# Performance work log

Hardware: AMD Instinct MI355X
Metric: run time of the kernel (lower is better)

Reference implementation:

```python
import jax, jax.numpy as jnp
import numpy as np

B, T, C = 4, 1024, 1024
N = 64          # head_size
H = C // N      # 16 heads
DW, DA, DV, DG = 64, 64, 64, 160


def setup_inputs() -> dict:
    key = jax.random.key(0)
    ks = iter(jax.random.split(key, 40))
    rn = lambda shape, s=1.0: jax.random.normal(next(ks), shape, dtype=jnp.float32) * s
    ru = lambda shape: jax.random.uniform(next(ks), shape, dtype=jnp.float32)
    cs = 0.5 / (C ** 0.5)
    return {
        "x": rn((B, T, C)),
        "v_first": rn((B, T, C)),
        "x_r": ru((1, 1, C)), "x_w": ru((1, 1, C)), "x_k": ru((1, 1, C)),
        "x_v": ru((1, 1, C)), "x_a": ru((1, 1, C)), "x_g": ru((1, 1, C)),
        "w0": rn((1, 1, C), 0.3) - 1.0,
        "w1": rn((C, DW), 0.05), "w2": rn((DW, C), 0.05),
        "a0": rn((1, 1, C), 0.3) - 0.19,
        "a1": rn((C, DA), 0.05), "a2": rn((DA, C), 0.05),
        "v0": rn((1, 1, C), 0.3) + 0.73,
        "v1": rn((C, DV), 0.05), "v2": rn((DV, C), 0.05),
        "g1": rn((C, DG), 0.05), "g2": rn((DG, C), 0.05),
        "k_k": ru((1, 1, C)) * 0.2 + 0.6,
        "k_a": ru((1, 1, C)) * 0.2 + 0.9,
        "r_k": rn((H, N), 0.05) - 0.04,
        "Wr": rn((C, C), cs), "Wk": rn((C, C), 0.1 * cs),
        "Wv": rn((C, C), cs), "Wo": rn((C, C), 0.02),
        "gn_w": jnp.ones((C,), jnp.float32), "gn_b": jnp.zeros((C,), jnp.float32),
        "ln_w": jnp.ones((C,), jnp.float32), "ln_b": jnp.zeros((C,), jnp.float32),
    }


def reference(x, v_first, x_r, x_w, x_k, x_v, x_a, x_g,
              w0, w1, w2, a0, a1, a2, v0, v1, v2, g1, g2,
              k_k, k_a, r_k, Wr, Wk, Wv, Wo, gn_w, gn_b, ln_w, ln_b):
    Bb, Tt, Cc = x.shape
    # ZeroPad2d((0,0,1,-1)): shift tokens right by one along T, then subtract x
    xx = jnp.concatenate([jnp.zeros_like(x[:, :1]), x[:, :-1]], axis=1) - x
    xr = x + xx * x_r; xw = x + xx * x_w; xkk = x + xx * x_k
    xv = x + xx * x_v; xa = x + xx * x_a; xg = x + xx * x_g

    r = xr @ Wr.T                                                    # [B,T,C]
    w = -jax.nn.softplus(-(w0 + jnp.tanh(xw @ w1) @ w2)) - 0.5       # log-decay <= -0.5
    k = xkk @ Wk.T
    v = xv @ Wv.T
    # layer_id=1 != 0 -> value residual mixing with v_first
    v = v + (v_first - v) * jax.nn.sigmoid(v0 + (xv @ v1) @ v2)
    a = jax.nn.sigmoid(a0 + (xa @ a1) @ a2)
    g = jax.nn.sigmoid(xg @ g1) @ g2

    kk = (k * k_k).reshape(Bb, Tt, H, N)
    kk = kk / jnp.maximum(jnp.linalg.norm(kk, axis=-1, keepdims=True), 1e-12)
    kk = kk.reshape(Bb, Tt, Cc)
    k = k * (1.0 + (a - 1.0) * k_a)

    # RWKV-7 generalized delta rule scan: kernel args (r, w, k, v, -kk, kk*a)
    decay = jnp.exp(-jnp.exp(w))                                     # [B,T,C]
    aa = -kk
    bb = kk * a
    tbhn = lambda t: t.reshape(Bb, Tt, H, N).transpose(1, 0, 2, 3)   # [T,B,H,N]
    rs, ws, ks_, vs, as_, bs = map(tbhn, (r, decay, k, v, aa, bb))

    S0 = jnp.zeros((Bb, H, N, N), dtype=x.dtype)  # [B,H, value N, key N]

    def step(S, inp):
        r_t, w_t, k_t, v_t, a_t, b_t = inp
        sa = jnp.einsum('bhij,bhj->bhi', S, a_t)                     # removal readout
        S = (S * w_t[:, :, None, :]
             + sa[..., None] * b_t[:, :, None, :]
             + v_t[..., None] * k_t[:, :, None, :])
        y = jnp.einsum('bhij,bhj->bhi', S, r_t)
        return S, (y, sa)

    _, (ys, sas) = jax.lax.scan(step, S0, (rs, ws, ks_, vs, as_, bs))
    x_att = ys.transpose(1, 0, 2, 3).reshape(Bb, Tt, Cc)
    sa_out = sas.transpose(1, 0, 2, 3).reshape(Bb, Tt, Cc)

    # ln_sa: LayerNorm over C (eps 1e-5)
    mu = sa_out.mean(-1, keepdims=True)
    var = sa_out.var(-1, keepdims=True)
    state_rep = (sa_out - mu) / jnp.sqrt(var + 1e-5) * ln_w + ln_b

    # ln_x: GroupNorm(H groups, eps=0.00064) applied per token
    xh = x_att.reshape(Bb, Tt, H, N)
    gm = xh.mean(-1, keepdims=True)
    gv = xh.var(-1, keepdims=True)
    xn = ((xh - gm) / jnp.sqrt(gv + 0.00064)).reshape(Bb, Tt, Cc) * gn_w + gn_b

    rh = r.reshape(Bb, Tt, H, N)
    kh = k.reshape(Bb, Tt, H, N)
    vh = v.reshape(Bb, Tt, H, N)
    bonus = ((rh * kh * r_k).sum(-1, keepdims=True) * vh).reshape(Bb, Tt, Cc)
    x_att = xn + bonus

    out = (x_att * g) @ Wo.T
    return out, v_first, state_rep
```

## Files before the change

### kernel.cpp

```cpp
#include <hip/hip_runtime.h>
#include <hip/hip_bf16.h>
#include <cstdint>
#include <cstddef>

typedef __attribute__((ext_vector_type(8))) short short8;
typedef __attribute__((ext_vector_type(4))) short short4v;
typedef __attribute__((ext_vector_type(4))) float f32x4;

#define DEVINL static __device__ __forceinline__

DEVINL float b2f(unsigned short u) {
    union { unsigned int i; float f; } v; v.i = ((unsigned int)u) << 16; return v.f;
}
DEVINL unsigned short f2bh(float f) {
    __hip_bfloat16 h = __float2bfloat16(f);
    union { __hip_bfloat16 h; unsigned short u; } v; v.h = h; return v.u;
}
DEVINL unsigned short f2b(float f) { return f2bh(f); }
DEVINL void cv8(short8 h, f32x4& lo, f32x4& hi) {
    #pragma unroll
    for (int j = 0; j < 4; ++j) {
        lo[j] = b2f((unsigned short)h[j]);
        hi[j] = b2f((unsigned short)h[j + 4]);
    }
}
DEVINL void cv4(short4v h, f32x4& o) {
    #pragma unroll
    for (int j = 0; j < 4; ++j) o[j] = b2f((unsigned short)h[j]);
}
DEVINL void stage16(const unsigned short* g, unsigned short* l) {
    __builtin_amdgcn_global_load_lds(
        (const __attribute__((address_space(1))) unsigned int*)g,
        (__attribute__((address_space(3))) unsigned int*)l,
        16, 0, 0);
}
DEVINL void xcd_swz(int& bx, int& by) {
    int id = by * 32 + bx;
    int k = id & 7, m = id >> 3;
    bx = 4 * k + (m & 3);
    by = m >> 2;
}

static constexpr int Bsz = 4, Tn = 1024, Cn = 1024, Hn = 16, Nn = 64;
static constexpr int Mrows = Bsz * Tn;
static constexpr size_t MX = (size_t)Mrows * Cn;
static constexpr int NCHUNK = 16, CL = 64;
static constexpr int DLD = 65;

__global__ __launch_bounds__(256) void k_prep_all(
    const float* __restrict__ x,
    const float* __restrict__ mr, const float* __restrict__ mw,
    const float* __restrict__ mk, const float* __restrict__ mv,
    const float* __restrict__ ma, const float* __restrict__ mg,
    unsigned short* __restrict__ xr, unsigned short* __restrict__ xw,
    unsigned short* __restrict__ xk, unsigned short* __restrict__ xv,
    unsigned short* __restrict__ xa, unsigned short* __restrict__ xg,
    const float* __restrict__ Wr, const float* __restrict__ Wk,
    const float* __restrict__ Wv, const float* __restrict__ Wo,
    unsigned short* __restrict__ WrB, unsigned short* __restrict__ WkB,
    unsigned short* __restrict__ WvB, unsigned short* __restrict__ WoB,
    const float* __restrict__ w1, const float* __restrict__ w2,
    const float* __restrict__ a1, const float* __restrict__ a2,
    const float* __restrict__ v1, const float* __restrict__ v2,
    const float* __restrict__ g1, const float* __restrict__ g2,
    unsigned short* __restrict__ w1T, unsigned short* __restrict__ w2T,
    unsigned short* __restrict__ a1T, unsigned short* __restrict__ a2T,
    unsigned short* __restrict__ v1T, unsigned short* __restrict__ v2T,
    unsigned short* __restrict__ g1T, unsigned short* __restrict__ g2T)
{
    const int bx = blockIdx.x;
    const int tid = threadIdx.x;
    if (bx < 2048) {
        size_t e = ((size_t)bx * 256 + tid) * 8;
        int c = (int)(e & (Cn - 1));
        int t = (int)((e >> 10) & (Tn - 1));
        float xf[8], d[8];
        {
            f32x4 x0 = *(const f32x4*)(x + e);
// ... 205 lines not shown
    if (b < 48) { zz = b >> 4; bxi = b & 15; byi = 0; }
    else        { zz = 3; int r = b - 48; bxi = r & 15; byi = r >> 4; }
    const unsigned short* A = (zz == 0) ? Aw : (zz == 1) ? Aa : (zz == 2) ? Avv : Ag;
    const unsigned short* Bt = (zz == 0) ? Bw1 : (zz == 1) ? Ba1 : (zz == 2) ? Bv1 : Bg1;
    const int N = (zz == 3) ? 160 : 64;
    const int tid = threadIdx.x, wid = tid >> 6, lane = tid & 63;
    const int r16 = lane & 15, k8 = (lane >> 4) * 8;
    const int m0 = bxi * 256 + wid * 64;
    const int n0 = byi * 64;
    f32x4 acc[4][4];
    #pragma unroll
    for (int a = 0; a < 4; ++a)
        #pragma unroll
        for (int bb = 0; bb < 4; ++bb) acc[a][bb] = (f32x4){0.f, 0.f, 0.f, 0.f};
    gemm_core(A, Cn, Bt, Cn, m0, n0, N, Cn, r16, k8, acc);
    if (zz == 0)      gemm_epi<1, 0>(acc, m0, n0, N, 64,  nullptr, Dw, nullptr, lane);
    else if (zz == 1) gemm_epi<0, 0>(acc, m0, n0, N, 64,  nullptr, Da, nullptr, lane);
    else if (zz == 2) gemm_epi<0, 0>(acc, m0, n0, N, 64,  nullptr, Dvh, nullptr, lane);
    else              gemm_epi<2, 0>(acc, m0, n0, N, 160, nullptr, Dg, nullptr, lane);
}

__global__ __launch_bounds__(256) void gemm_s2(
    const unsigned short* __restrict__ hw, const unsigned short* __restrict__ ha,
    const unsigned short* __restrict__ hv, const unsigned short* __restrict__ hg,
    const unsigned short* __restrict__ w2T, const unsigned short* __restrict__ a2T,
    const unsigned short* __restrict__ v2T, const unsigned short* __restrict__ g2T,
    float* __restrict__ Wdec, unsigned short* __restrict__ Ab,
    unsigned short* __restrict__ SVb, unsigned short* __restrict__ Gb,
    const float* __restrict__ w0, const float* __restrict__ a0,
    const float* __restrict__ v0)
{
    const int z = blockIdx.z;
    int bxs = blockIdx.x, bys = blockIdx.y;
    xcd_swz(bxs, bys);
    const int m0 = bxs * 128, n0 = bys * 128;
    if (z == 0)
        gemm_lds_body<4, 1>(hw, 64, w2T, 64, Wdec, nullptr, Cn, w0, 64, m0, n0);
    else if (z == 1)
        gemm_lds_body<3, 0>(ha, 64, a2T, 64, nullptr, Ab, Cn, a0, 64, m0, n0);
    else if (z == 2)
        gemm_lds_body<3, 0>(hv, 64, v2T, 64, nullptr, SVb, Cn, v0, 64, m0, n0);
    else
        gemm_lds_body<0, 0>(hg, 160, g2T, 160, nullptr, Gb, Cn, nullptr, 160, m0, n0);
}

__global__ __launch_bounds__(1024, 1) void kA_wy(
    const float* __restrict__ Wp,
    unsigned short* __restrict__ Kp,
    unsigned short* __restrict__ Vp,
    const unsigned short* __restrict__ SVp,
    unsigned short* __restrict__ Aap,
    const float* __restrict__ vfirst,
    const float* __restrict__ kkw, const float* __restrict__ kaw,
    float* __restrict__ Pg,
    float* __restrict__ Cg,
    float* __restrict__ Qg,
    float* __restrict__ SAp)
{
    __shared__ float Dl[64 * DLD];
    __shared__ float Lf[64 * 72];
    __shared__ float Xf[64 * 132];
    __shared__ unsigned short ah[64 * 72], al[64 * 72];
    __shared__ unsigned short bh_[64 * 72], bl_[64 * 72];
    __shared__ unsigned short kh[64 * 72], kl[64 * 72];
    __shared__ unsigned short vt[64 * 72];
    __shared__ unsigned short sc[64 * 72];
    __shared__ float dT[64];

    const int tid = threadIdx.x;
    const int bx = blockIdx.x;
    const int bhd = bx >> 4, cc = bx & 15;
    const size_t base0 = ((size_t)(bhd >> 4) * Tn + (size_t)cc * CL) * Cn + (size_t)(bhd & 15) * Nn;
    const size_t mb = (size_t)bx * 4096;

    {
        const int t = tid >> 4, s4 = (tid & 15) * 4;
        const size_t g = base0 + (size_t)t * Cn + s4;
        const int ch = (bhd & 15) * Nn + s4;

        f32x4 kv, av, vv, sv;
        cv4(*(const short4v*)(Kp + g), kv);
        cv4(*(const short4v*)(Aap + g), av);
        cv4(*(const short4v*)(Vp + g), vv);
        cv4(*(const short4v*)(SVp + g), sv);
        f32x4 kkwv = *(const f32x4*)(kkw + ch);
        f32x4 kawv = *(const f32x4*)(kaw + ch);
        f32x4 vfv  = *(const f32x4*)(vfirst + g);

        f32x4 kkv = kv * kkwv;
        f32x4 sq = kkv * kkv;
        float s = sq[0] + sq[1] + sq[2] + sq[3];
        s += __shfl_xor(s, 1, 64); s += __shfl_xor(s, 2, 64);
        s += __shfl_xor(s, 4, 64); s += __shfl_xor(s, 8, 64);
        float inv = 1.f / fmaxf(sqrtf(s), 1e-12f);

        short4v o_a, o_b, o_k, o_v;
        #pragma unroll
        for (int j = 0; j < 4; ++j) {
            float kkx = kkv[j] * inv;
            o_a[j] = (short)f2b(-kkx);
            o_b[j] = (short)f2b(kkx * av[j]);
            float kf = kv[j] * (1.f + (av[j] - 1.f) * kawv[j]);
            o_k[j] = (short)f2b(kf);
            float vf = vv[j] + (vfv[j] - vv[j]) * sv[j];
            o_v[j] = (short)f2b(vf);
        }
        *(short4v*)&ah[t * 72 + s4] = o_a;
        *(short4v*)&bh_[t * 72 + s4] = o_b;
        *(short4v*)&kh[t * 72 + s4] = o_k;
// ... 109 lines not shown
        for (int jj = 0; jj < 4; ++jj)
            Xf[t * 132 + s4 + jj] = b2f(ah[t * 72 + s4 + jj]) + b2f(al[t * 72 + s4 + jj]);
    }
    {
        f32x4 acc = (f32x4){0.f, 0.f, 0.f, 0.f};
        #pragma unroll
        for (int ks = 0; ks < 2; ++ks) {
            short8 Af = *(const short8*)&sc[(rt * 16 + r16) * 72 + ks * 32 + kg * 8];
            short8 Bf = *(const short8*)&vt[(ct * 16 + r16) * 72 + ks * 32 + kg * 8];
            acc = __builtin_amdgcn_mfma_f32_16x16x32_bf16(Af, Bf, acc, 0, 0, 0);
        }
        #pragma unroll
        for (int r = 0; r < 4; ++r)
            Xf[(rt * 16 + kg * 4 + r) * 132 + 64 + ct * 16 + r16] = acc[r];
    }
    __syncthreads();

    for (int bi = 0; bi < 4; ++bi) {
        if (bi > 0) {
            const int c = tid & 127;
            const int rb = tid >> 7;
            const int t0 = bi * 16 + rb * 2;
            float a0 = Xf[t0 * 132 + c];
            float a1 = Xf[(t0 + 1) * 132 + c];
            for (int s = 0; s < bi * 16; ++s) {
                float xv = Xf[s * 132 + c];
                a0 += Lf[t0 * 72 + s] * xv;
                a1 += Lf[(t0 + 1) * 72 + s] * xv;
            }
            Xf[t0 * 132 + c] = a0;
            Xf[(t0 + 1) * 132 + c] = a1;
            __syncthreads();
        }
        if (w < 2) {
            const int c = w * 64 + lane;
            float xcol[16];
            #pragma unroll
            for (int u = 0; u < 16; ++u) xcol[u] = Xf[(bi * 16 + u) * 132 + c];
            for (int rr = 1; rr < 16; ++rr) {
                float a2 = xcol[rr];
                for (int s = 0; s < rr; ++s)
                    a2 += Lf[(bi * 16 + rr) * 72 + bi * 16 + s] * xcol[s];
                xcol[rr] = a2;
            }
            #pragma unroll
            for (int u = 1; u < 16; ++u) Xf[(bi * 16 + u) * 132 + c] = xcol[u];
        }
        __syncthreads();
    }

    {
        const int rj = tid & 63, tq = tid >> 6;
        float qv[4], sv[4];
        unsigned short bhv[4], blv[4], khv[4], klv[4];
        #pragma unroll
        for (int u = 0; u < 4; ++u) {
            const int t = tq * 4 + u;
            qv[u] = Xf[t * 132 + rj];
            sv[u] = Xf[t * 132 + 64 + rj];
            bhv[u] = bh_[t * 72 + rj];
            blv[u] = bl_[t * 72 + rj];
            khv[u] = kh[t * 72 + rj];
            klv[u] = kl[t * 72 + rj];
        }
        #pragma unroll
        for (int u = 0; u < 4; ++u) {
            const int t = tq * 4 + u;
            Qg[mb + (size_t)t * 64 + rj] = qv[u];
            SAp[base0 + (size_t)t * Cn + rj] = sv[u];
        }
        __syncthreads();
        unsigned short* sath = (unsigned short*)Lf;
        unsigned short* satl = ((unsigned short*)Lf) + 64 * 72;
        short4v oqh, oql, osh, osl, obh, obl, okh, okl;
        #pragma unroll
        for (int u = 0; u < 4; ++u) {
            unsigned short h = f2bh(qv[u]);
            oqh[u] = (short)h; oql[u] = (short)f2bh(qv[u] - b2f(h));
            h = f2bh(sv[u]);
            osh[u] = (short)h; osl[u] = (short)f2bh(sv[u] - b2f(h));
            obh[u] = (short)bhv[u]; obl[u] = (short)blv[u];
            okh[u] = (short)khv[u]; okl[u] = (short)klv[u];
        }
        *(short4v*)&ah[rj * 72 + tq * 4] = oqh;
        *(short4v*)&al[rj * 72 + tq * 4] = oql;
        *(short4v*)&sath[rj * 72 + tq * 4] = osh;
        *(short4v*)&satl[rj * 72 + tq * 4] = osl;
        *(short4v*)&bh_[rj * 72 + tq * 4] = obh;
        *(short4v*)&bl_[rj * 72 + tq * 4] = obl;
        *(short4v*)&kh[rj * 72 + tq * 4] = okh;
        *(short4v*)&kl[rj * 72 + tq * 4] = okl;
    }
    __syncthreads();

    {
        unsigned short* sath = (unsigned short*)Lf;
        unsigned short* satl = ((unsigned short*)Lf) + 64 * 72;
        f32x4 aP = (f32x4){0.f, 0.f, 0.f, 0.f};
        f32x4 aC = (f32x4){0.f, 0.f, 0.f, 0.f};
        #pragma unroll
        for (int ks = 0; ks < 2; ++ks) {
            const int ro = (rt * 16 + r16) * 72 + ks * 32 + kg * 8;
            const int co = (ct * 16 + r16) * 72 + ks * 32 + kg * 8;
            short8 Abh = *(const short8*)&bh_[ro];
            short8 Abl = *(const short8*)&bl_[ro];
            short8 Bqh = *(const short8*)&ah[co];
            short8 Bql = *(const short8*)&al[co];
            aP = __builtin_amdgcn_mfma_f32_16x16x32_bf16(Abh, Bqh, aP, 0, 0, 0);
            aP = __builtin_amdgcn_mfma_f32_16x16x32_bf16(Abh, Bql, aP, 0, 0, 0);
            aP = __builtin_amdgcn_mfma_f32_16x16x32_bf16(Abl, Bqh, aP, 0, 0, 0);
            short8 Ash = *(const short8*)&sath[ro];
            short8 Asl = *(const short8*)&satl[ro];
            short8 Bbh = *(const short8*)&bh_[co];
            short8 Bbl = *(const short8*)&bl_[co];
            aC = __builtin_amdgcn_mfma_f32_16x16x32_bf16(Ash, Bbh, aC, 0, 0, 0);
            aC = __builtin_amdgcn_mfma_f32_16x16x32_bf16(Ash, Bbl, aC, 0, 0, 0);
            aC = __builtin_amdgcn_mfma_f32_16x16x32_bf16(Asl, Bbh, aC, 0, 0, 0);
            short8 Avt = *(const short8*)&vt[ro];
            short8 Bkh = *(const short8*)&kh[co];
            short8 Bkl = *(const short8*)&kl[co];
            aC = __builtin_amdgcn_mfma_f32_16x16x32_bf16(Avt, Bkh, aC, 0, 0, 0);
            aC = __builtin_amdgcn_mfma_f32_16x16x32_bf16(Avt, Bkl, aC, 0, 0, 0);
        }
        #pragma unroll
        for (int r = 0; r < 4; ++r) {
            const int row = rt * 16 + kg * 4 + r;
            const int col = ct * 16 + r16;
            Pg[mb + (size_t)row * 64 + col] = dT[row] * (aP[r] + ((row == col) ? 1.f : 0.f));
            Cg[mb + (size_t)row * 64 + col] = dT[col] * aC[r];
        }
    }
}

__global__ __launch_bounds__(256, 1) void kB_combine(
    const float* __restrict__ Pg, const float* __restrict__ Cg,
    float* __restrict__ Sinit)
{
    __shared__ float Sl[64 * 65];
    __shared__ float PT[64 * 65];
    const int tid = threadIdx.x;
    const int w = tid >> 6;
    const int l = tid & 63;
    const int lr = l & 15;
    const int lg = l >> 4;
    const int bh = blockIdx.x;

    f32x4 acc[4];
    #pragma unroll
    for (int t = 0; t < 4; ++t) acc[t] = (f32x4){0.f, 0.f, 0.f, 0.f};

    f32x4 pr[4]; f32x4 cr[4];
    {
        const size_t ob = (size_t)(bh * 16) * 4096;
        #pragma unroll
        for (int u = 0; u < 4; ++u)
            pr[u] = *(const f32x4*)(Pg + ob + (size_t)tid * 16 + u * 4);
        #pragma unroll
        for (int t = 0; t < 4; ++t)
            #pragma unroll
            for (int r = 0; r < 4; ++r)
                cr[t][r] = Cg[ob + (size_t)(16 * w + 4 * lg + r) * 64 + 16 * t + lr];
    }

    for (int c = 0; c < NCHUNK; ++c) {
        const size_t ob = (size_t)(bh * 16 + c) * 4096;
        #pragma unroll
        for (int t = 0; t < 4; ++t)
            #pragma unroll
            for (int r = 0; r < 4; ++r)
                Sinit[ob + (size_t)(16 * w + 4 * lg + r) * 64 + 16 * t + lr] = acc[t][r];
        if (c == NCHUNK - 1) break;

        #pragma unroll
        for (int t = 0; t < 4; ++t)
            #pragma unroll
            for (int r = 0; r < 4; ++r)
                Sl[(16 * w + 4 * lg + r) * 65 + 16 * t + lr] = acc[t][r];
        {
            const int jr = tid >> 2, j0 = (tid & 3) * 16;
            #pragma unroll
            for (int u = 0; u < 4; ++u)
                #pragma unroll
                for (int e = 0; e < 4; ++e)
                    PT[jr * 65 + j0 + u * 4 + e] = pr[u][e];
        }
        __syncthreads();

        f32x4 prn[4] = {}, crn[4] = {};
        if (c + 1 < NCHUNK - 1) {
            const size_t obn = (size_t)(bh * 16 + c + 1) * 4096;
            #pragma unroll
            for (int u = 0; u < 4; ++u)
                prn[u] = *(const f32x4*)(Pg + obn + (size_t)tid * 16 + u * 4);
            #pragma unroll
            for (int t = 0; t < 4; ++t)
                #pragma unroll
                for (int r = 0; r < 4; ++r)
                    crn[t][r] = Cg[obn + (size_t)(16 * w + 4 * lg + r) * 64 + 16 * t + lr];
        }

        short8 ahi[2], alo[2];
        #pragma unroll
        for (int k0 = 0; k0 < 2; ++k0) {
            const float* sp = &Sl[(16 * w + lr) * 65 + k0 * 32 + lg * 8];
            #pragma unroll
            for (int j = 0; j < 8; ++j) {
                float s = sp[j];
                unsigned short h = f2bh(s);
                ahi[k0][j] = (short)h;
                alo[k0][j] = (short)f2bh(s - b2f(h));
            }
        }

        #pragma unroll
        for (int t = 0; t < 4; ++t) {
            f32x4 nacc = cr[t];
            #pragma unroll
            for (int k0 = 0; k0 < 2; ++k0) {
                short8 bhi, blo;
                const float* pp = &PT[(16 * t + lr) * 65 + k0 * 32 + lg * 8];
                #pragma unroll
                for (int j = 0; j < 8; ++j) {
                    float p = pp[j];
                    unsigned short h = f2bh(p);
                    bhi[j] = (short)h;
                    blo[j] = (short)f2bh(p - b2f(h));
                }
                nacc = __builtin_amdgcn_mfma_f32_16x16x32_bf16(ahi[k0], bhi, nacc, 0, 0, 0);
                nacc = __builtin_amdgcn_mfma_f32_16x16x32_bf16(ahi[k0], blo, nacc, 0, 0, 0);
                nacc = __builtin_amdgcn_mfma_f32_16x16x32_bf16(alo[k0], bhi, nacc, 0, 0, 0);
            }
            acc[t] = nacc;
        }
        __syncthreads();
        #pragma unroll
        for (int u = 0; u < 4; ++u) { pr[u] = prn[u]; cr[u] = crn[u]; }
    }
}

__global__ __launch_bounds__(256) void kY_mfma(
    const float* __restrict__ Wp, const unsigned short* __restrict__ Rp,
    const unsigned short* __restrict__ Kp, const unsigned short* __restrict__ Bbp,
    const unsigned short* __restrict__ Vp, const unsigned short* __restrict__ Gb,
    const float* __restrict__ Qg, const float* __restrict__ Sinit,
    const float* __restrict__ gnw, const float* __restrict__ gnb,
    const float* __restrict__ rk,
    float* __restrict__ SAp,
    unsigned short* __restrict__ AG)
{
    __shared__ float Dl[64 * DLD];
    __shared__ unsigned short khS[64 * 72], klS[64 * 72];
    __shared__ unsigned short bhS[64 * 72], blS[64 * 72];
    __shared__ unsigned short vtS[64 * 72];
    __shared__ unsigned short sahS[64 * 72];

    unsigned short* scoreS = (unsigned short*)Dl;
    float* SAf = Dl;
    float* segP = (float*)vtS;

    const int tid = threadIdx.x;
    const int bx = blockIdx.x;
    const int bh = bx >> 4, cc = bx & 15;
    const size_t base0 = ((size_t)(bh >> 4) * Tn + (size_t)cc * CL) * Cn + (size_t)(bh & 15) * Nn;
    const size_t mb = (size_t)bx * 4096;

    float wv[16];
    {
        const int j = tid & 63, seg = tid >> 6;
        float run = 1.f;
        #pragma unroll
        for (int u = 0; u < 16; ++u) {
            wv[u] = Wp[base0 + (size_t)(seg * 16 + u) * Cn + j];
            run *= wv[u];
        }
        segP[seg * 64 + j] = run;
    }
    __syncthreads();
    {
        const int j = tid & 63, seg = tid >> 6;
        float d = 1.f;
        for (int q = 0; q < seg; ++q) d *= segP[q * 64 + j];
        #pragma unroll
        for (int u = 0; u < 16; ++u) {
            d *= wv[u];
            Dl[(seg * 16 + u) * DLD + j] = d;
        }
    }
    __syncthreads();

    const int w = tid >> 6, lane = tid & 63;
    const int r16 = lane & 15, kg = lane >> 4;

    short8 rh[2], rl[2];
    {
        const int t = 16 * w + r16;
        #pragma unroll
        for (int ks = 0; ks < 2; ++ks) {
// ... 15 lines not shown
        const size_t g = base0 + (size_t)s * Cn + j0;
        #pragma unroll
        for (int half = 0; half < 2; ++half) {
            short8 kk8 = *(const short8*)(Kp + g + half * 8);
            short8 bb8 = *(const short8*)(Bbp + g + half * 8);
            short8 okh, okl, obh, obl;
            #pragma unroll
            for (int jj = 0; jj < 8; ++jj) {
                float dd = Dl[s * DLD + j0 + half * 8 + jj];
                float inv = __builtin_amdgcn_rcpf(dd);
                float kv = b2f((unsigned short)kk8[jj]) * inv;
                float bv = b2f((unsigned short)bb8[jj]) * inv;
                unsigned short h1 = f2bh(kv);
                okh[jj] = (short)h1; okl[jj] = (short)f2bh(kv - b2f(h1));
                unsigned short h2 = f2bh(bv);
                obh[jj] = (short)h2; obl[jj] = (short)f2bh(bv - b2f(h2));
            }
            *(short8*)&khS[s * 72 + j0 + half * 8] = okh;
            *(short8*)&klS[s * 72 + j0 + half * 8] = okl;
            *(short8*)&bhS[s * 72 + j0 + half * 8] = obh;
            *(short8*)&blS[s * 72 + j0 + half * 8] = obl;
            *(short8*)&sahS[s * 72 + j0 + half * 8] =
                *(const short8*)(Vp + g + half * 8);
        }
    }
    __syncthreads();

    {
        const int rj = tid & 63, tq = tid >> 6;
        unsigned short tmp[16];
        #pragma unroll
        for (int u = 0; u < 16; ++u)
            tmp[u] = sahS[(tq * 16 + u) * 72 + rj];
        short8 o0, o1;
        #pragma unroll
        for (int u = 0; u < 8; ++u) { o0[u] = (short)tmp[u]; o1[u] = (short)tmp[8 + u]; }
        *(short8*)&vtS[rj * 72 + tq * 16] = o0;
        *(short8*)&vtS[rj * 72 + tq * 16 + 8] = o1;
    }
    __syncthreads();

    f32x4 acc[4], accC[4];
    #pragma unroll
    for (int ni = 0; ni < 4; ++ni) {
        acc[ni] = (f32x4){0.f, 0.f, 0.f, 0.f};
        accC[ni] = (f32x4){0.f, 0.f, 0.f, 0.f};
    }
    short8 qh[2], ql[2];
    if (cc > 0) {
        const int t = 16 * w + r16;
        #pragma unroll
        for (int ks = 0; ks < 2; ++ks) {
            const int j0 = ks * 32 + kg * 8;
            f32x4 qa = *(const f32x4*)(Qg + mb + (size_t)t * 64 + j0);
            f32x4 qb = *(const f32x4*)(Qg + mb + (size_t)t * 64 + j0 + 4);
            #pragma unroll
            for (int jj = 0; jj < 4; ++jj) {
                unsigned short h1 = f2bh(qa[jj]);
                qh[ks][jj] = (short)h1; ql[ks][jj] = (short)f2bh(qa[jj] - b2f(h1));
                unsigned short h2 = f2bh(qb[jj]);
                qh[ks][4 + jj] = (short)h2; ql[ks][4 + jj] = (short)f2bh(qb[jj] - b2f(h2));
            }
        }
    }
    #pragma unroll
    for (int ni = 0; ni < 4; ++ni) {
        #pragma unroll
        for (int ks = 0; ks < 2; ++ks) {
            const int i = ni * 16 + r16;
            const int j0 = ks * 32 + kg * 8;
            f32x4 s0a = *(const f32x4*)(Sinit + mb + (size_t)i * 64 + j0);
            f32x4 s0b = *(const f32x4*)(Sinit + mb + (size_t)i * 64 + j0 + 4);
            short8 s0h, s0l;
            #pragma unroll
            for (int jj = 0; jj < 4; ++jj) {
                unsigned short h1 = f2bh(s0a[jj]);
                s0h[jj] = (short)h1; s0l[jj] = (short)f2bh(s0a[jj] - b2f(h1));
                unsigned short h2 = f2bh(s0b[jj]);
                s0h[4 + jj] = (short)h2; s0l[4 + jj] = (short)f2bh(s0b[jj] - b2f(h2));
            }
            acc[ni] = __builtin_amdgcn_mfma_f32_16x16x32_bf16(rh[ks], s0h, acc[ni], 0, 0, 0);
            acc[ni] = __builtin_amdgcn_mfma_f32_16x16x32_bf16(rh[ks], s0l, acc[ni], 0, 0, 0);
            acc[ni] = __builtin_amdgcn_mfma_f32_16x16x32_bf16(rl[ks], s0h, acc[ni], 0, 0, 0);
            if (cc > 0) {
                accC[ni] = __builtin_amdgcn_mfma_f32_16x16x32_bf16(qh[ks], s0h, accC[ni], 0, 0, 0);
                accC[ni] = __builtin_amdgcn_mfma_f32_16x16x32_bf16(qh[ks], s0l, accC[ni], 0, 0, 0);
                accC[ni] = __builtin_amdgcn_mfma_f32_16x16x32_bf16(ql[ks], s0h, accC[ni], 0, 0, 0);
            }
        }
    }

    #pragma unroll
    for (int ni = 0; ni < 4; ++ni) {
        #pragma unroll
        for (int r = 0; r < 4; ++r) {
            const int t = 16 * w + kg * 4 + r;
            const int i = ni * 16 + r16;
            const size_t off = base0 + (size_t)t * Cn + i;
            float sa = SAp[off] + accC[ni][r];
            SAp[off] = sa;
            SAf[t * 65 + i] = sa;
        }
    }
    __syncthreads();

    {
        const int rj = tid & 63, tq = tid >> 6;
        unsigned short tmp[16];
        #pragma unroll
        for (int u = 0; u < 16; ++u)
            tmp[u] = f2bh(SAf[(tq * 16 + u) * 65 + rj]);
        short8 o0, o1;
        #pragma unroll
        for (int u = 0; u < 8; ++u) { o0[u] = (short)tmp[u]; o1[u] = (short)tmp[8 + u]; }
        *(short8*)&sahS[rj * 72 + tq * 16] = o0;
        *(short8*)&sahS[rj * 72 + tq * 16 + 8] = o1;
    }
    __syncthreads();

    #pragma unroll
    for (int si = 0; si < 4; ++si) {
        f32x4 sc2 = (f32x4){0.f, 0.f, 0.f, 0.f};
        #pragma unroll
        for (int ks = 0; ks < 2; ++ks) {
            const int srow = si * 16 + r16;
            const int j0 = ks * 32 + kg * 8;
            short8 kbh = *(const short8*)&khS[srow * 72 + j0];
            short8 kbl = *(const short8*)&klS[srow * 72 + j0];
            sc2 = __builtin_amdgcn_mfma_f32_16x16x32_bf16(rh[ks], kbh, sc2, 0, 0, 0);
            sc2 = __builtin_amdgcn_mfma_f32_16x16x32_bf16(rh[ks], kbl, sc2, 0, 0, 0);
            sc2 = __builtin_amdgcn_mfma_f32_16x16x32_bf16(rl[ks], kbh, sc2, 0, 0, 0);
        }
        const int s = si * 16 + r16;
// ... 53 lines not shown
            rkv[ni] = rk[c]; gnwv[ni] = gnw[c]; gnbv[ni] = gnb[c];
        }
        #pragma unroll
        for (int r = 0; r < 4; ++r) {
            const int t = 16 * w + kg * 4 + r;
            const size_t rowb = base0 + (size_t)t * Cn;
            float s1 = 0.f, s2 = 0.f, p = 0.f;
            float yv[4];
            #pragma unroll
            for (int ni = 0; ni < 4; ++ni) {
                float y = acc[ni][r];
                yv[ni] = y;
                s1 += y; s2 += y * y;
                const int i = ni * 16 + r16;
                p += b2f(Rp[rowb + i]) * b2f(Kp[rowb + i]) * rkv[ni];
            }
            s1 += __shfl_xor(s1, 1, 64); s1 += __shfl_xor(s1, 2, 64);
            s1 += __shfl_xor(s1, 4, 64); s1 += __shfl_xor(s1, 8, 64);
            s2 += __shfl_xor(s2, 1, 64); s2 += __shfl_xor(s2, 2, 64);
            s2 += __shfl_xor(s2, 4, 64); s2 += __shfl_xor(s2, 8, 64);
            p  += __shfl_xor(p, 1, 64);  p  += __shfl_xor(p, 2, 64);
            p  += __shfl_xor(p, 4, 64);  p  += __shfl_xor(p, 8, 64);
            float mean = s1 * (1.f / 64.f);
            float var = s2 * (1.f / 64.f) - mean * mean;
            float rs = rsqrtf(var + 0.00064f);
            #pragma unroll
            for (int ni = 0; ni < 4; ++ni) {
                const int i = ni * 16 + r16;
                float xn = (yv[ni] - mean) * rs * gnwv[ni] + gnbv[ni];
                float vv2 = b2f(vtS[i * 72 + t]);
                float xatt = xn + p * vv2;
                float gv = b2f(Gb[rowb + i]);
                AG[rowb + i] = f2b(xatt * gv);
            }
        }
    }
}

__global__ __launch_bounds__(256) void k_back(
    const unsigned short* __restrict__ AG, const unsigned short* __restrict__ WoB,
    float* __restrict__ out_o,
    const float* __restrict__ SAp,
    const float* __restrict__ lnw, const float* __restrict__ lnb,
    const float* __restrict__ vf_in, float* __restrict__ vf_out,
    float* __restrict__ outp)
{
    if (blockIdx.z == 0) {
        int bxs = blockIdx.x, bys = blockIdx.y;
        xcd_swz(bxs, bys);
        gemm_lds_body<0, 1>(AG, Cn, WoB, Cn, out_o, nullptr, Cn, nullptr, Cn,
                            bxs * 128, bys * 128);
        return;
    }
    __shared__ float red1[4], red2[4];
    const int tid = threadIdx.x;
    const int fb = blockIdx.y * 32 + blockIdx.x;
    for (int rr = 0; rr < 16; ++rr) {
        size_t row = (size_t)fb * 16 + rr;
        *(f32x4*)(vf_out + row * Cn + tid * 4) = *(const f32x4*)(vf_in + row * Cn + tid * 4);

        f32x4 v = *(const f32x4*)(SAp + row * Cn + tid * 4);
        float s1 = v[0] + v[1] + v[2] + v[3];
        float s2 = v[0] * v[0] + v[1] * v[1] + v[2] * v[2] + v[3] * v[3];
        #pragma unroll
        for (int m = 1; m < 64; m <<= 1) {
            s1 += __shfl_xor(s1, m, 64);
            s2 += __shfl_xor(s2, m, 64);
        }
        if ((tid & 63) == 0) { red1[tid >> 6] = s1; red2[tid >> 6] = s2; }
        __syncthreads();
        s1 = red1[0] + red1[1] + red1[2] + red1[3];
        s2 = red2[0] + red2[1] + red2[2] + red2[3];
        float mean = s1 * (1.f / 1024.f);
        float var = s2 * (1.f / 1024.f) - mean * mean;
        float rs = rsqrtf(var + 1e-5f);
        f32x4 o;
        #pragma unroll
        for (int u = 0; u < 4; ++u) {
            int c = tid * 4 + u;
            o[u] = (v[u] - mean) * rs * lnw[c] + lnb[c];
        }
        *(f32x4*)(outp + row * Cn + tid * 4) = o;
        __syncthreads();
    }
}

extern "C" void kernel_launch(void* const* d_in, const int* in_sizes, int n_in,
                              void* d_out, int out_size, void* d_ws, size_t ws_size,
                              hipStream_t stream)
{
    (void)in_sizes; (void)n_in; (void)out_size; (void)ws_size;
    const float* x      = (const float*)d_in[0];
    const float* vfirst = (const float*)d_in[1];
    const float* x_r    = (const float*)d_in[2];
    const float* x_w    = (const float*)d_in[3];
    const float* x_k    = (const float*)d_in[4];
    const float* x_v    = (const float*)d_in[5];
    const float* x_a    = (const float*)d_in[6];
    const float* x_g    = (const float*)d_in[7];
    const float* w0     = (const float*)d_in[8];
    const float* w1     = (const float*)d_in[9];
    const float* w2     = (const float*)d_in[10];
    const float* a0     = (const float*)d_in[11];
    const float* a1     = (const float*)d_in[12];
    const float* a2     = (const float*)d_in[13];
    const float* v0     = (const float*)d_in[14];
    const float* v1     = (const float*)d_in[15];
    const float* v2     = (const float*)d_in[16];
    const float* g1     = (const float*)d_in[17];
    const float* g2     = (const float*)d_in[18];
    const float* k_k    = (const float*)d_in[19];
    const float* k_a    = (const float*)d_in[20];
    const float* r_k    = (const float*)d_in[21];
    const float* Wr     = (const float*)d_in[22];
    const float* Wk     = (const float*)d_in[23];
    const float* Wv     = (const float*)d_in[24];
    const float* Wo     = (const float*)d_in[25];
    const float* gn_w   = (const float*)d_in[26];
    const float* gn_b   = (const float*)d_in[27];
    const float* ln_w   = (const float*)d_in[28];
    const float* ln_b   = (const float*)d_in[29];

    char* ws = (char*)d_ws;
    size_t off = 0;
    auto alloc = [&](size_t bytes) -> void* {
        void* p = ws + off;
        off += (bytes + 255) & ~(size_t)255;
        return p;
    };
    unsigned short* Rb  = (unsigned short*)alloc(MX * 2);
    unsigned short* Kb  = (unsigned short*)alloc(MX * 2);
    unsigned short* Vb  = (unsigned short*)alloc(MX * 2);
    unsigned short* SVb = (unsigned short*)alloc(MX * 2);
    unsigned short* Ab  = (unsigned short*)alloc(MX * 2);
    unsigned short* Gb  = (unsigned short*)alloc(MX * 2);
    float* Wdec = (float*)alloc(MX * 4);
    float* Cg   = (float*)alloc(MX * 4);
    float* Pg   = (float*)alloc(MX * 4);
    float* Qg   = (float*)alloc(MX * 4);
    unsigned short* hw = (unsigned short*)alloc((size_t)Mrows * 64 * 2);
    unsigned short* ha = (unsigned short*)alloc((size_t)Mrows * 64 * 2);
    unsigned short* hv = (unsigned short*)alloc((size_t)Mrows * 64 * 2);
    unsigned short* hg = (unsigned short*)alloc((size_t)Mrows * 160 * 2);
    unsigned short* WrB = (unsigned short*)alloc(1048576 * 2);
    unsigned short* WkB = (unsigned short*)alloc(1048576 * 2);
    unsigned short* WvB = (unsigned short*)alloc(1048576 * 2);
    unsigned short* WoB = (unsigned short*)alloc(1048576 * 2);
    unsigned short* w1T = (unsigned short*)alloc(65536 * 2);
    unsigned short* w2T = (unsigned short*)alloc(65536 * 2);
    unsigned short* a1T = (unsigned short*)alloc(65536 * 2);
    unsigned short* a2T = (unsigned short*)alloc(65536 * 2);
    unsigned short* v1T = (unsigned short*)alloc(65536 * 2);
    unsigned short* v2T = (unsigned short*)alloc(65536 * 2);
    unsigned short* g1T = (unsigned short*)alloc(163840 * 2);
    unsigned short* g2T = (unsigned short*)alloc(163840 * 2);

    unsigned short* xrB = (unsigned short*)Cg;
    unsigned short* xkB = (unsigned short*)Cg + MX;
    unsigned short* xvB = (unsigned short*)Wdec;
    unsigned short* xgB = (unsigned short*)Wdec + MX;
    unsigned short* xwB = Ab;
    unsigned short* xaB = Gb;

    float* out_o  = (float*)d_out;
    float* out_vf = out_o + MX;
    float* out_sr = out_o + 2 * MX;
    float* Sinit = out_vf;
    float* SAb   = out_sr;
    unsigned short* AG = Rb;

    k_prep_all<<<dim3(8960), 256, 0, stream>>>(
        x, x_r, x_w, x_k, x_v, x_a, x_g,
        xrB, xwB, xkB, xvB, xaB, xgB,
        Wr, Wk, Wv, Wo, WrB, WkB, WvB, WoB,
        w1, w2, a1, a2, v1, v2, g1, g2,
        w1T, w2T, a1T, a2T, v1T, v2T, g1T, g2T);

    gemm_front<<<dim3(864), 256, 0, stream>>>(
        xrB, xkB, xvB, WrB, WkB, WvB, Rb, Kb, Vb,
        xwB, xaB, xgB, w1T, a1T, v1T, g1T,
        hw, ha, hv, hg);

    gemm_s2<<<dim3(32, 8, 4), 256, 0, stream>>>(hw, ha, hv, hg,
                                                w2T, a2T, v2T, g2T,
                                                Wdec, Ab, SVb, Gb,
                                                w0, a0, v0);

    kA_wy<<<dim3(1024), 1024, 0, stream>>>(Wdec, Kb, Vb, SVb, Ab,
                                           vfirst, k_k, k_a,
                                           Pg, Cg, Qg, SAb);
    kB_combine<<<dim3(64), 256, 0, stream>>>(Pg, Cg, Sinit);
    kY_mfma<<<dim3(1024), 256, 0, stream>>>(Wdec, Rb, Kb, Ab, Vb, Gb,
                                            Qg, Sinit, gn_w, gn_b, r_k,
                                            SAb, AG);

    k_back<<<dim3(32, 8, 2), 256, 0, stream>>>(AG, WoB, out_o,
                                               SAb, ln_w, ln_b,
                                               vfirst, out_vf, out_sr);
}
```

Measured before the change: 269.5 us.

## Store P, Q, S as hi/lo bf16 pairs and split combine K across waves

```diff
diff --git a/kernel.cpp b/kernel.cpp
--- a/kernel.cpp
+++ b/kernel.cpp
@@ -17,13 +17,6 @@
     union { __hip_bfloat16 h; unsigned short u; } v; v.h = h; return v.u;
 }
 DEVINL unsigned short f2b(float f) { return f2bh(f); }
-DEVINL void cv8(short8 h, f32x4& lo, f32x4& hi) {
-    #pragma unroll
-    for (int j = 0; j < 4; ++j) {
-        lo[j] = b2f((unsigned short)h[j]);
-        hi[j] = b2f((unsigned short)h[j + 4]);
-    }
-}
 DEVINL void cv4(short4v h, f32x4& o) {
     #pragma unroll
     for (int j = 0; j < 4; ++j) o[j] = b2f((unsigned short)h[j]);
@@ -335,9 +328,9 @@
     unsigned short* __restrict__ Aap,
     const float* __restrict__ vfirst,
     const float* __restrict__ kkw, const float* __restrict__ kaw,
-    float* __restrict__ Pg,
+    unsigned short* __restrict__ Phi, unsigned short* __restrict__ Plo,
     float* __restrict__ Cg,
-    float* __restrict__ Qg,
+    unsigned short* __restrict__ Qhi, unsigned short* __restrict__ Qlo,
     float* __restrict__ SAp)
 {
     __shared__ float Dl[64 * DLD];
@@ -553,6 +546,7 @@
     {
         const int rj = tid & 63, tq = tid >> 6;
         float qv[4], sv[4];
+        unsigned short qhv[4], qlv[4];
         unsigned short bhv[4], blv[4], khv[4], klv[4];
         #pragma unroll
         for (int u = 0; u < 4; ++u) {
@@ -567,7 +561,10 @@
         #pragma unroll
         for (int u = 0; u < 4; ++u) {
             const int t = tq * 4 + u;
-            Qg[mb + (size_t)t * 64 + rj] = qv[u];
+            qhv[u] = f2bh(qv[u]);
+            qlv[u] = f2bh(qv[u] - b2f(qhv[u]));
+            Qhi[mb + (size_t)t * 64 + rj] = qhv[u];
+            Qlo[mb + (size_t)t * 64 + rj] = qlv[u];
             SAp[base0 + (size_t)t * Cn + rj] = sv[u];
         }
         __syncthreads();
@@ -576,9 +573,8 @@
         short4v oqh, oql, osh, osl, obh, obl, okh, okl;
         #pragma unroll
         for (int u = 0; u < 4; ++u) {
-            unsigned short h = f2bh(qv[u]);
-            oqh[u] = (short)h; oql[u] = (short)f2bh(qv[u] - b2f(h));
-            h = f2bh(sv[u]);
+            oqh[u] = (short)qhv[u]; oql[u] = (short)qlv[u];
+            unsigned short h = f2bh(sv[u]);
             osh[u] = (short)h; osl[u] = (short)f2bh(sv[u] - b2f(h));
             obh[u] = (short)bhv[u]; obl[u] = (short)blv[u];
             okh[u] = (short)khv[u]; okl[u] = (short)klv[u];
@@ -627,115 +623,111 @@
         for (int r = 0; r < 4; ++r) {
             const int row = rt * 16 + kg * 4 + r;
             const int col = ct * 16 + r16;
-            Pg[mb + (size_t)row * 64 + col] = dT[row] * (aP[r] + ((row == col) ? 1.f : 0.f));
+            float pv = dT[row] * (aP[r] + ((row == col) ? 1.f : 0.f));
+            unsigned short ph = f2bh(pv);
+            Phi[mb + (size_t)row * 64 + col] = ph;
+            Plo[mb + (size_t)row * 64 + col] = f2bh(pv - b2f(ph));
             Cg[mb + (size_t)row * 64 + col] = dT[col] * aC[r];
         }
     }
 }
 
-__global__ __launch_bounds__(256, 1) void kB_combine(
-    const float* __restrict__ Pg, const float* __restrict__ Cg,
-    float* __restrict__ Sinit)
+__global__ __launch_bounds__(512, 1) void kB_combine(
+    const unsigned short* __restrict__ Phi, const unsigned short* __restrict__ Plo,
+    const float* __restrict__ Cg,
+    unsigned short* __restrict__ Shi, unsigned short* __restrict__ Slo)
 {
     __shared__ float Sl[64 * 65];
-    __shared__ float PT[64 * 65];
+    __shared__ float Pp[64 * 65];
     const int tid = threadIdx.x;
-    const int w = tid >> 6;
+    const int w2 = tid >> 6;
+    const int rb = w2 & 3, kh2 = w2 >> 2;
     const int l = tid & 63;
-    const int lr = l & 15;
-    const int lg = l >> 4;
+    const int lr = l & 15, lg = l >> 4;
     const int bh = blockIdx.x;
 
     f32x4 acc[4];
     #pragma unroll
     for (int t = 0; t < 4; ++t) acc[t] = (f32x4){0.f, 0.f, 0.f, 0.f};
 
-    f32x4 pr[4]; f32x4 cr[4];
-    {
+    f32x4 cr[4];
+    if (kh2 == 0) {
         const size_t ob = (size_t)(bh * 16) * 4096;
         #pragma unroll
-        for (int u = 0; u < 4; ++u)
-            pr[u] = *(const f32x4*)(Pg + ob + (size_t)tid * 16 + u * 4);
-        #pragma unroll
         for (int t = 0; t < 4; ++t)
             #pragma unroll
             for (int r = 0; r < 4; ++r)
-                cr[t][r] = Cg[ob + (size_t)(16 * w + 4 * lg + r) * 64 + 16 * t + lr];
+                cr[t][r] = Cg[ob + (size_t)(16 * rb + 4 * lg + r) * 64 + 16 * t + lr];
     }
 
     for (int c = 0; c < NCHUNK; ++c) {
         const size_t ob = (size_t)(bh * 16 + c) * 4096;
-        #pragma unroll
-        for (int t = 0; t < 4; ++t)
-            #pragma unroll
-            for (int r = 0; r < 4; ++r)
-                Sinit[ob + (size_t)(16 * w + 4 * lg + r) * 64 + 16 * t + lr] = acc[t][r];
+        if (kh2 == 0) {
+            #pragma unroll
+            for (int t = 0; t < 4; ++t)
+                #pragma unroll
+                for (int r = 0; r < 4; ++r) {
+                    const int row = 16 * rb + 4 * lg + r;
+                    const int col = 16 * t + lr;
+                    float s = acc[t][r];
+                    unsigned short h = f2bh(s);
+                    Shi[ob + (size_t)row * 64 + col] = h;
+                    Slo[ob + (size_t)row * 64 + col] = f2bh(s - b2f(h));
+                    Sl[row * 65 + col] = s;
+                }
+        }
         if (c == NCHUNK - 1) break;
-
-        #pragma unroll
-        for (int t = 0; t < 4; ++t)
-            #pragma unroll
-            for (int r = 0; r < 4; ++r)
-                Sl[(16 * w + 4 * lg + r) * 65 + 16 * t + lr] = acc[t][r];
+        __syncthreads();
+
+        short8 ahi, alo;
         {
-            const int jr = tid >> 2, j0 = (tid & 3) * 16;
-            #pragma unroll
-            for (int u = 0; u < 4; ++u)
-                #pragma unroll
-                for (int e = 0; e < 4; ++e)
-                    PT[jr * 65 + j0 + u * 4 + e] = pr[u][e];
-        }
-        __syncthreads();
-
-        f32x4 prn[4] = {}, crn[4] = {};
-        if (c + 1 < NCHUNK - 1) {
-            const size_t obn = (size_t)(bh * 16 + c + 1) * 4096;
-            #pragma unroll
-            for (int u = 0; u < 4; ++u)
-                prn[u] = *(const f32x4*)(Pg + obn + (size_t)tid * 16 + u * 4);
+            const float* sp = &Sl[(16 * rb + lr) * 65 + kh2 * 32 + lg * 8];
+            #pragma unroll
+            for (int j = 0; j < 8; ++j) {
+                float s = sp[j];
+                unsigned short h = f2bh(s);
+                ahi[j] = (short)h;
+                alo[j] = (short)f2bh(s - b2f(h));
+            }
+        }
+
+        f32x4 pacc[4];
+        #pragma unroll
+        for (int t = 0; t < 4; ++t) {
+            const size_t po = ob + (size_t)(16 * t + lr) * 64 + kh2 * 32 + lg * 8;
+            short8 bhi = *(const short8*)&Phi[po];
+            short8 blo = *(const short8*)&Plo[po];
+            f32x4 nacc = (kh2 == 0) ? cr[t] : (f32x4){0.f, 0.f, 0.f, 0.f};
+            nacc = __builtin_amdgcn_mfma_f32_16x16x32_bf16(ahi, bhi, nacc, 0, 0, 0);
+            nacc = __builtin_amdgcn_mfma_f32_16x16x32_bf16(ahi, blo, nacc, 0, 0, 0);
+            nacc = __builtin_amdgcn_mfma_f32_16x16x32_bf16(alo, bhi, nacc, 0, 0, 0);
+            pacc[t] = nacc;
+        }
+
+        if (kh2 == 1) {
             #pragma unroll
             for (int t = 0; t < 4; ++t)
                 #pragma unroll
                 for (int r = 0; r < 4; ++r)
-                    crn[t][r] = Cg[obn + (size_t)(16 * w + 4 * lg + r) * 64 + 16 * t + lr];
-        }
-
-        short8 ahi[2], alo[2];
-        #pragma unroll
-        for (int k0 = 0; k0 < 2; ++k0) {
-            const float* sp = &Sl[(16 * w + lr) * 65 + k0 * 32 + lg * 8];
-            #pragma unroll
-            for (int j = 0; j < 8; ++j) {
-                float s = sp[j];
-                unsigned short h = f2bh(s);
-                ahi[k0][j] = (short)h;
-                alo[k0][j] = (short)f2bh(s - b2f(h));
-            }
-        }
-
-        #pragma unroll
-        for (int t = 0; t < 4; ++t) {
-            f32x4 nacc = cr[t];
-            #pragma unroll
-            for (int k0 = 0; k0 < 2; ++k0) {
-                short8 bhi, blo;
-                const float* pp = &PT[(16 * t + lr) * 65 + k0 * 32 + lg * 8];
+                    Pp[(16 * rb + 4 * lg + r) * 65 + 16 * t + lr] = pacc[t][r];
+        }
+        __syncthreads();
+        if (kh2 == 0) {
+            #pragma unroll
+            for (int t = 0; t < 4; ++t)
                 #pragma unroll
-                for (int j = 0; j < 8; ++j) {
-                    float p = pp[j];
-                    unsigned short h = f2bh(p);
-                    bhi[j] = (short)h;
-                    blo[j] = (short)f2bh(p - b2f(h));
-                }
-                nacc = __builtin_amdgcn_mfma_f32_16x16x32_bf16(ahi[k0], bhi, nacc, 0, 0, 0);
-                nacc = __builtin_amdgcn_mfma_f32_16x16x32_bf16(ahi[k0], blo, nacc, 0, 0, 0);
-                nacc = __builtin_amdgcn_mfma_f32_16x16x32_bf16(alo[k0], bhi, nacc, 0, 0, 0);
-            }
-            acc[t] = nacc;
+                for (int r = 0; r < 4; ++r)
+                    acc[t][r] = pacc[t][r] + Pp[(16 * rb + 4 * lg + r) * 65 + 16 * t + lr];
+            if (c + 1 < NCHUNK - 1) {
+                const size_t obn = (size_t)(bh * 16 + c + 1) * 4096;
+                #pragma unroll
+                for (int t = 0; t < 4; ++t)
+                    #pragma unroll
+                    for (int r = 0; r < 4; ++r)
+                        cr[t][r] = Cg[obn + (size_t)(16 * rb + 4 * lg + r) * 64 + 16 * t + lr];
+            }
         }
         __syncthreads();
-        #pragma unroll
-        for (int u = 0; u < 4; ++u) { pr[u] = prn[u]; cr[u] = crn[u]; }
     }
 }
 
@@ -743,7 +735,8 @@
     const float* __restrict__ Wp, const unsigned short* __restrict__ Rp,
     const unsigned short* __restrict__ Kp, const unsigned short* __restrict__ Bbp,
     const unsigned short* __restrict__ Vp, const unsigned short* __restrict__ Gb,
-    const float* __restrict__ Qg, const float* __restrict__ Sinit,
+    const unsigned short* __restrict__ Qhi, const unsigned short* __restrict__ Qlo,
+    const unsigned short* __restrict__ Shi, const unsigned short* __restrict__ Slo,
     const float* __restrict__ gnw, const float* __restrict__ gnb,
     const float* __restrict__ rk,
     float* __restrict__ SAp,
@@ -865,15 +858,8 @@
         #pragma unroll
         for (int ks = 0; ks < 2; ++ks) {
             const int j0 = ks * 32 + kg * 8;
-            f32x4 qa = *(const f32x4*)(Qg + mb + (size_t)t * 64 + j0);
-            f32x4 qb = *(const f32x4*)(Qg + mb + (size_t)t * 64 + j0 + 4);
-            #pragma unroll
-            for (int jj = 0; jj < 4; ++jj) {
-                unsigned short h1 = f2bh(qa[jj]);
-                qh[ks][jj] = (short)h1; ql[ks][jj] = (short)f2bh(qa[jj] - b2f(h1));
-                unsigned short h2 = f2bh(qb[jj]);
-                qh[ks][4 + jj] = (short)h2; ql[ks][4 + jj] = (short)f2bh(qb[jj] - b2f(h2));
-            }
+            qh[ks] = *(const short8*)&Qhi[mb + (size_t)t * 64 + j0];
+            ql[ks] = *(const short8*)&Qlo[mb + (size_t)t * 64 + j0];
         }
     }
     #pragma unroll
@@ -882,16 +868,8 @@
         for (int ks = 0; ks < 2; ++ks) {
             const int i = ni * 16 + r16;
             const int j0 = ks * 32 + kg * 8;
-            f32x4 s0a = *(const f32x4*)(Sinit + mb + (size_t)i * 64 + j0);
-            f32x4 s0b = *(const f32x4*)(Sinit + mb + (size_t)i * 64 + j0 + 4);
-            short8 s0h, s0l;
-            #pragma unroll
-            for (int jj = 0; jj < 4; ++jj) {
-                unsigned short h1 = f2bh(s0a[jj]);
-                s0h[jj] = (short)h1; s0l[jj] = (short)f2bh(s0a[jj] - b2f(h1));
-                unsigned short h2 = f2bh(s0b[jj]);
-                s0h[4 + jj] = (short)h2; s0l[4 + jj] = (short)f2bh(s0b[jj] - b2f(h2));
-            }
+            short8 s0h = *(const short8*)&Shi[mb + (size_t)i * 64 + j0];
+            short8 s0l = *(const short8*)&Slo[mb + (size_t)i * 64 + j0];
             acc[ni] = __builtin_amdgcn_mfma_f32_16x16x32_bf16(rh[ks], s0h, acc[ni], 0, 0, 0);
             acc[ni] = __builtin_amdgcn_mfma_f32_16x16x32_bf16(rh[ks], s0l, acc[ni], 0, 0, 0);
             acc[ni] = __builtin_amdgcn_mfma_f32_16x16x32_bf16(rl[ks], s0h, acc[ni], 0, 0, 0);
@@ -1051,36 +1029,40 @@
                             bxs * 128, bys * 128);
         return;
     }
-    __shared__ float red1[4], red2[4];
     const int tid = threadIdx.x;
+    const int wv = tid >> 6, l = tid & 63;
     const int fb = blockIdx.y * 32 + blockIdx.x;
-    for (int rr = 0; rr < 16; ++rr) {
-        size_t row = (size_t)fb * 16 + rr;
-        *(f32x4*)(vf_out + row * Cn + tid * 4) = *(const f32x4*)(vf_in + row * Cn + tid * 4);
-
-        f32x4 v = *(const f32x4*)(SAp + row * Cn + tid * 4);
-        float s1 = v[0] + v[1] + v[2] + v[3];
-        float s2 = v[0] * v[0] + v[1] * v[1] + v[2] * v[2] + v[3] * v[3];
+    for (int rr = 0; rr < 4; ++rr) {
+        size_t row = (size_t)fb * 16 + wv * 4 + rr;
+        const size_t rb = row * Cn;
+        f32x4 v[4];
+        float s1 = 0.f, s2 = 0.f;
+        #pragma unroll
+        for (int p = 0; p < 4; ++p) {
+            const size_t o = rb + p * 256 + l * 4;
+            v[p] = *(const f32x4*)(SAp + o);
+            *(f32x4*)(vf_out + o) = *(const f32x4*)(vf_in + o);
+            #pragma unroll
+            for (int u = 0; u < 4; ++u) { s1 += v[p][u]; s2 += v[p][u] * v[p][u]; }
+        }
         #pragma unroll
         for (int m = 1; m < 64; m <<= 1) {
             s1 += __shfl_xor(s1, m, 64);
             s2 += __shfl_xor(s2, m, 64);
         }
-        if ((tid & 63) == 0) { red1[tid >> 6] = s1; red2[tid >> 6] = s2; }
-        __syncthreads();
-        s1 = red1[0] + red1[1] + red1[2] + red1[3];
-        s2 = red2[0] + red2[1] + red2[2] + red2[3];
         float mean = s1 * (1.f / 1024.f);
         float var = s2 * (1.f / 1024.f) - mean * mean;
         float rs = rsqrtf(var + 1e-5f);
-        f32x4 o;
-        #pragma unroll
-        for (int u = 0; u < 4; ++u) {
-            int c = tid * 4 + u;
-            o[u] = (v[u] - mean) * rs * lnw[c] + lnb[c];
-        }
-        *(f32x4*)(outp + row * Cn + tid * 4) = o;
-        __syncthreads();
+        #pragma unroll
+        for (int p = 0; p < 4; ++p) {
+            f32x4 o;
+            #pragma unroll
+            for (int u = 0; u < 4; ++u) {
+                int c = p * 256 + l * 4 + u;
+                o[u] = (v[p][u] - mean) * rs * lnw[c] + lnb[c];
+            }
+            *(f32x4*)(outp + rb + p * 256 + l * 4) = o;
+        }
     }
 }
 
@@ -1154,6 +1136,11 @@
     unsigned short* g1T = (unsigned short*)alloc(163840 * 2);
     unsigned short* g2T = (unsigned short*)alloc(163840 * 2);
 
+    unsigned short* Phi = (unsigned short*)Pg;
+    unsigned short* Plo = Phi + MX;
+    unsigned short* Qhi = (unsigned short*)Qg;
+    unsigned short* Qlo = Qhi + MX;
+
     unsigned short* xrB = (unsigned short*)Cg;
     unsigned short* xkB = (unsigned short*)Cg + MX;
     unsigned short* xvB = (unsigned short*)Wdec;
@@ -1164,7 +1151,8 @@
     float* out_o  = (float*)d_out;
     float* out_vf = out_o + MX;
     float* out_sr = out_o + 2 * MX;
-    float* Sinit = out_vf;
+    unsigned short* Shi = (unsigned short*)out_vf;
+    unsigned short* Slo = Shi + MX;
     float* SAb   = out_sr;
     unsigned short* AG = Rb;
 
@@ -1187,10 +1175,11 @@
 
     kA_wy<<<dim3(1024), 1024, 0, stream>>>(Wdec, Kb, Vb, SVb, Ab,
                                            vfirst, k_k, k_a,
-                                           Pg, Cg, Qg, SAb);
-    kB_combine<<<dim3(64), 256, 0, stream>>>(Pg, Cg, Sinit);
+                                           Phi, Plo, Cg, Qhi, Qlo, SAb);
+    kB_combine<<<dim3(64), 512, 0, stream>>>(Phi, Plo, Cg, Shi, Slo);
     kY_mfma<<<dim3(1024), 256, 0, stream>>>(Wdec, Rb, Kb, Ab, Vb, Gb,
-                                            Qg, Sinit, gn_w, gn_b, r_k,
+                                            Qhi, Qlo, Shi, Slo,
+                                            gn_w, gn_b, r_k,
                                             SAb, AG);
 
     k_back<<<dim3(32, 8, 2), 256, 0, stream>>>(AG, WoB, out_o,
```

New measurement: 291.3 us. +8.1%, slower.
